# Optimization experiments

Hardware: AMD Instinct MI355X
Metric: run time of the kernel (lower is better)

Reference implementation:

```python
import jax, jax.numpy as jnp
import numpy as np

SCENE = (60, 36, 60)          # int(4.8/0.08), int(2.88/0.08), int(4.8/0.08)
VOX = 0.08
DS = 4
IMG_W, IMG_H = 640, 480
N_VOX = SCENE[0] * SCENE[1] * SCENE[2]

def _voxel_grid():
    gx, gy, gz = np.meshgrid(np.arange(SCENE[0]), np.arange(SCENE[1]), np.arange(SCENE[2]), indexing='ij')
    return np.stack([gx.ravel(), gy.ravel(), gz.ravel()], axis=1).astype(np.float32)  # [N,3]

_GRID = jnp.asarray(_voxel_grid())


def setup_inputs() -> dict:
    key = jax.random.key(0)
    x2d = jax.random.normal(jax.random.fold_in(key, 0), (512, IMG_H // DS, IMG_W // DS), dtype=jnp.float32)
    inv_cam_pose = jnp.eye(4, dtype=jnp.float32)
    vox_origin = jnp.array([-2.4, -2.4, 0.1], dtype=jnp.float32)
    cam_k = jnp.array([[518.8579, 0.0, 320.0], [0.0, 518.8579, 240.0], [0.0, 0.0, 1.0]], dtype=jnp.float32)
    old_voxel_indices = jax.random.randint(jax.random.fold_in(key, 1), (1000, 3), 0, 60)
    old_image_indices = jax.random.randint(jax.random.fold_in(key, 2), (1000, 2), 0, 480)
    return {"x2d": x2d, "inv_cam_pose": inv_cam_pose, "vox_origin": vox_origin, "cam_k": cam_k,
            "old_voxel_indices": old_voxel_indices, "old_image_indices": old_image_indices, "fliplr": 0}


def reference(x2d, inv_cam_pose, vox_origin, cam_k, old_voxel_indices, old_image_indices, fliplr):
    # old_voxel_indices / old_image_indices are unused in the original forward.
    c, h, w = x2d.shape
    grid = _GRID                                        # [N,3] voxel integer coords (float)
    pts_world2 = grid * VOX + 0.5 * VOX                 # voxel centers
    # axis swap: world (x, z, y) then shift by origin
    pts_world = jnp.stack([pts_world2[:, 0], pts_world2[:, 2], pts_world2[:, 1]], axis=1) + vox_origin[None, :]
    homo = jnp.concatenate([pts_world, jnp.ones((pts_world.shape[0], 1), pts_world.dtype)], axis=1)
    pts_cam = homo @ inv_cam_pose.T                     # [N,4] camera frame
    in_front = pts_cam[:, 2] > 0
    pts_img = pts_cam[:, :3] @ cam_k.T                  # [N,3]
    uv = jnp.round(pts_img[:, :2] / pts_img[:, 2:3])    # [N,2] = (x_col, y_row)
    in_frustum = (uv[:, 0] >= 0) & (uv[:, 0] < IMG_W) & (uv[:, 1] >= 0) & (uv[:, 1] < IMG_H)
    mask = in_front & in_frustum

    row, col = uv[:, 1], uv[:, 0]                       # torch.fliplr -> (y, x)
    if fliplr:
        col = IMG_W - 1 - col
    row = jnp.floor(row / DS)                           # // downsample
    col = jnp.floor(col / DS)
    lin_img = jnp.where(mask, (row * w + col), 0.0).astype(jnp.int32)  # safe gather index

    src = x2d.reshape(c, -1)
    feats = src[:, lin_img]                             # [c, N] gather

    lin_vox = (grid[:, 0] * (SCENE[1] * SCENE[2]) + grid[:, 1] * SCENE[2] + grid[:, 2]).astype(jnp.int32)
    lin_vox = jnp.where(mask, lin_vox, N_VOX)           # out-of-range -> dropped
    x3d = jnp.zeros((c, N_VOX), x2d.dtype).at[:, lin_vox].set(feats, mode='drop')
    return x3d.reshape(c, SCENE[0], SCENE[1], SCENE[2])
```

## Files before the change

kernel.cpp:

```cpp
#include <hip/hip_runtime.h>

#define NVOX 129600
#define NCH  512
#define IMH  120
#define IMW  160
#define NPIX (IMH * IMW)
#define LSTRIDE 161
#define PLANE_LDS (IMH * LSTRIDE)

typedef float vfloat4 __attribute__((ext_vector_type(4)));

__device__ __forceinline__ int project_voxel_pad(
    int v, const float* __restrict__ pose, const float* __restrict__ origin,
    const float* __restrict__ camk, int flip)
{
    int gx = v / 2160;
    int r  = v - gx * 2160;
    int gy = r / 60;
    int gz = r - gy * 60;
    float wx = gx * 0.08f + 0.04f + origin[0];
    float wy = gz * 0.08f + 0.04f + origin[1];
    float wz = gy * 0.08f + 0.04f + origin[2];
    float cx = pose[0]*wx + pose[1]*wy + pose[2]*wz  + pose[3];
    float cy = pose[4]*wx + pose[5]*wy + pose[6]*wz  + pose[7];
    float cz = pose[8]*wx + pose[9]*wy + pose[10]*wz + pose[11];
    float ix = camk[0]*cx + camk[1]*cy + camk[2]*cz;
    float iy = camk[3]*cx + camk[4]*cy + camk[5]*cz;
    float iz = camk[6]*cx + camk[7]*cy + camk[8]*cz;
    float u  = rintf(ix / iz);
    float vv = rintf(iy / iz);
    bool ok = (cz > 0.0f) && (u >= 0.0f) && (u < 640.0f)
                          && (vv >= 0.0f) && (vv < 480.0f);
    if (!ok) return -1;
    float colf = flip ? (639.0f - u) : u;
    return (((int)vv) >> 2) * LSTRIDE + (((int)colf) >> 2);
}

__global__ __launch_bounds__(256) void proj_kernel(
    int* __restrict__ lin,
    const float* __restrict__ pose, const float* __restrict__ origin,
    const float* __restrict__ camk, const int* __restrict__ fliplr)
{
    int v = blockIdx.x * 256 + threadIdx.x;
    if (v < NVOX)
        lin[v] = project_voxel_pad(v, pose, origin, camk, fliplr[0]);
}

__global__ __launch_bounds__(1024, 8) void chan_kernel(
    const float* __restrict__ x2d, const int* __restrict__ lin,
    float* __restrict__ out)
{
    __shared__ float plane[PLANE_LDS];
    int c = blockIdx.x;
    int t = threadIdx.x;

    const float4* src4 = reinterpret_cast<const float4*>(x2d)
                       + (size_t)c * (NPIX / 4);
#pragma unroll
    for (int i = 0; i < 5; ++i) {
        int p4 = i * 1024 + t;
        if (p4 < NPIX / 4) {
            float4 val = src4[p4];
            int p   = p4 * 4;
            int row = p / IMW;
            int col = p - row * IMW;
            float* d = &plane[row * LSTRIDE + col];
            d[0] = val.x; d[1] = val.y; d[2] = val.z; d[3] = val.w;
        }
    }
    __syncthreads();

    const int4* lin4 = reinterpret_cast<const int4*>(lin);
    vfloat4* out4 = reinterpret_cast<vfloat4*>(out) + (size_t)c * (NVOX / 4);
#pragma unroll 4
    for (int i = 0; i < 32; ++i) {
        int g = i * 1024 + t;
        if (g < NVOX / 4) {
            int4 l = lin4[g];
            vfloat4 o;
            o.x = (l.x >= 0) ? plane[l.x] : 0.0f;
            o.y = (l.y >= 0) ? plane[l.y] : 0.0f;
            o.z = (l.z >= 0) ? plane[l.z] : 0.0f;
            o.w = (l.w >= 0) ? plane[l.w] : 0.0f;
            __builtin_nontemporal_store(o, &out4[g]);
        }
    }
}

__global__ __launch_bounds__(256) void fused_kernel(
    const float* __restrict__ x2d, const float* __restrict__ pose,
    const float* __restrict__ origin, const float* __restrict__ camk,
    const int* __restrict__ fliplr, float* __restrict__ out)
{
    long tid = (long)blockIdx.x * blockDim.x + threadIdx.x;
    int g  = (int)(tid % 32400);
    int cg = (int)(tid / 32400);
    if (cg >= 64) return;
    int v0 = g * 4;
    int linv[4];
#pragma unroll
    for (int i = 0; i < 4; ++i) {
        int lp = project_voxel_pad(v0 + i, pose, origin, camk, fliplr[0]);
        linv[i] = (lp >= 0) ? (lp - lp / LSTRIDE) : -1;
    }
    int ch0 = cg * 8;
#pragma unroll
    for (int cc = 0; cc < 8; ++cc) {
        int ch = ch0 + cc;
        const float* s = x2d + (size_t)ch * NPIX;
        float4 o;
        o.x = (linv[0] >= 0) ? s[linv[0]] : 0.0f;
        o.y = (linv[1] >= 0) ? s[linv[1]] : 0.0f;
        o.z = (linv[2] >= 0) ? s[linv[2]] : 0.0f;
        o.w = (linv[3] >= 0) ? s[linv[3]] : 0.0f;
        *reinterpret_cast<float4*>(out + (size_t)ch * NVOX + v0) = o;
    }
}

extern "C" void kernel_launch(void* const* d_in, const int* in_sizes, int n_in,
                              void* d_out, int out_size, void* d_ws, size_t ws_size,
                              hipStream_t stream) {
    const float* x2d    = (const float*)d_in[0];
    const float* pose   = (const float*)d_in[1];
    const float* origin = (const float*)d_in[2];
    const float* camk   = (const float*)d_in[3];
    const int*   flip   = (const int*)d_in[6];
    float*       out    = (float*)d_out;

    const size_t lin_bytes = (size_t)NVOX * sizeof(int);
    if (ws_size >= lin_bytes) {
        int* linb = (int*)d_ws;
        proj_kernel<<<dim3((NVOX + 255) / 256), dim3(256), 0, stream>>>(
            linb, pose, origin, camk, flip);
        chan_kernel<<<dim3(NCH), dim3(1024), 0, stream>>>(x2d, linb, out);
    } else {
        fused_kernel<<<dim3(8100), dim3(256), 0, stream>>>(
            x2d, pose, origin, camk, flip, out);
    }
}
```

Before: 65.52 us.

## Process two channels per block with interleaved LDS plane and 16-bit indices

The channel kernel now handles two channels per block. It interleaves both planes into LDS as float2 pairs so that one LDS read serves both outputs, and it reuses each index load across two channels. Projection indices are stored as 16-bit values, which halves index traffic, and the plane loads use nontemporal loads. In exchange LDS use doubles to about 155KB per block and only 256 blocks are launched, so occupancy and wave-level parallelism drop.

New measurement: 63.66 us. 2.8% less time.

```diff
diff --git a/kernel.cpp b/kernel.cpp
--- a/kernel.cpp
+++ b/kernel.cpp
@@ -5,14 +5,16 @@
 #define IMH  120
 #define IMW  160
 #define NPIX (IMH * IMW)
-#define LSTRIDE 161
-#define PLANE_LDS (IMH * LSTRIDE)
+#define LSTR2 162
+#define PLANE2 (IMH * LSTR2)
 
 typedef float vfloat4 __attribute__((ext_vector_type(4)));
+typedef float vfloat2 __attribute__((ext_vector_type(2)));
+typedef unsigned short vushort4 __attribute__((ext_vector_type(4)));
 
-__device__ __forceinline__ int project_voxel_pad(
+__device__ __forceinline__ int project_voxel_s(
     int v, const float* __restrict__ pose, const float* __restrict__ origin,
-    const float* __restrict__ camk, int flip)
+    const float* __restrict__ camk, int flip, int stride)
 {
     int gx = v / 2160;
     int r  = v - gx * 2160;
@@ -33,56 +35,71 @@
                           && (vv >= 0.0f) && (vv < 480.0f);
     if (!ok) return -1;
     float colf = flip ? (639.0f - u) : u;
-    return (((int)vv) >> 2) * LSTRIDE + (((int)colf) >> 2);
+    return (((int)vv) >> 2) * stride + (((int)colf) >> 2);
 }
 
 __global__ __launch_bounds__(256) void proj_kernel(
-    int* __restrict__ lin,
+    unsigned short* __restrict__ lin16,
     const float* __restrict__ pose, const float* __restrict__ origin,
     const float* __restrict__ camk, const int* __restrict__ fliplr)
 {
     int v = blockIdx.x * 256 + threadIdx.x;
-    if (v < NVOX)
-        lin[v] = project_voxel_pad(v, pose, origin, camk, fliplr[0]);
+    if (v < NVOX) {
+        int l = project_voxel_s(v, pose, origin, camk, fliplr[0], LSTR2);
+        lin16[v] = (l >= 0) ? (unsigned short)l : (unsigned short)0xFFFF;
+    }
 }
 
-__global__ __launch_bounds__(1024, 8) void chan_kernel(
-    const float* __restrict__ x2d, const int* __restrict__ lin,
+__global__ __launch_bounds__(1024, 1) void chan2_kernel(
+    const float* __restrict__ x2d, const unsigned short* __restrict__ lin16,
     float* __restrict__ out)
 {
-    __shared__ float plane[PLANE_LDS];
-    int c = blockIdx.x;
+    __shared__ vfloat2 plane[PLANE2];
+    int b = blockIdx.x;
     int t = threadIdx.x;
+    int c0 = b * 2;
 
-    const float4* src4 = reinterpret_cast<const float4*>(x2d)
-                       + (size_t)c * (NPIX / 4);
+    const vfloat4* srcA = reinterpret_cast<const vfloat4*>(
+        x2d + (size_t)c0 * NPIX);
+    const vfloat4* srcB = reinterpret_cast<const vfloat4*>(
+        x2d + (size_t)(c0 + 1) * NPIX);
 #pragma unroll
     for (int i = 0; i < 5; ++i) {
-        int p4 = i * 1024 + t;
-        if (p4 < NPIX / 4) {
-            float4 val = src4[p4];
-            int p   = p4 * 4;
+        int j = i * 1024 + t;
+        if (j < NPIX / 4) {
+            vfloat4 a  = __builtin_nontemporal_load(&srcA[j]);
+            vfloat4 b4 = __builtin_nontemporal_load(&srcB[j]);
+            int p   = j * 4;
             int row = p / IMW;
             int col = p - row * IMW;
-            float* d = &plane[row * LSTRIDE + col];
-            d[0] = val.x; d[1] = val.y; d[2] = val.z; d[3] = val.w;
+            int idx = row * LSTR2 + col;
+            vfloat4 w0 = {a.x, b4.x, a.y, b4.y};
+            vfloat4 w1 = {a.z, b4.z, a.w, b4.w};
+            *reinterpret_cast<vfloat4*>(&plane[idx])     = w0;
+            *reinterpret_cast<vfloat4*>(&plane[idx + 2]) = w1;
         }
     }
     __syncthreads();
 
-    const int4* lin4 = reinterpret_cast<const int4*>(lin);
-    vfloat4* out4 = reinterpret_cast<vfloat4*>(out) + (size_t)c * (NVOX / 4);
+    vfloat4* outA = reinterpret_cast<vfloat4*>(out + (size_t)c0 * NVOX);
+    vfloat4* outB = reinterpret_cast<vfloat4*>(out + (size_t)(c0 + 1) * NVOX);
 #pragma unroll 4
     for (int i = 0; i < 32; ++i) {
         int g = i * 1024 + t;
         if (g < NVOX / 4) {
-            int4 l = lin4[g];
-            vfloat4 o;
-            o.x = (l.x >= 0) ? plane[l.x] : 0.0f;
-            o.y = (l.y >= 0) ? plane[l.y] : 0.0f;
-            o.z = (l.z >= 0) ? plane[l.z] : 0.0f;
-            o.w = (l.w >= 0) ? plane[l.w] : 0.0f;
-            __builtin_nontemporal_store(o, &out4[g]);
+            vushort4 l4 = *reinterpret_cast<const vushort4*>(lin16 + g * 4);
+            bool m0 = l4.x != 0xFFFFu, m1 = l4.y != 0xFFFFu,
+                 m2 = l4.z != 0xFFFFu, m3 = l4.w != 0xFFFFu;
+            vfloat2 v0 = plane[m0 ? l4.x : 0];
+            vfloat2 v1 = plane[m1 ? l4.y : 0];
+            vfloat2 v2 = plane[m2 ? l4.z : 0];
+            vfloat2 v3 = plane[m3 ? l4.w : 0];
+            vfloat4 oA = { m0 ? v0.x : 0.0f, m1 ? v1.x : 0.0f,
+                           m2 ? v2.x : 0.0f, m3 ? v3.x : 0.0f };
+            vfloat4 oB = { m0 ? v0.y : 0.0f, m1 ? v1.y : 0.0f,
+                           m2 ? v2.y : 0.0f, m3 ? v3.y : 0.0f };
+            __builtin_nontemporal_store(oA, &outA[g]);
+            __builtin_nontemporal_store(oB, &outB[g]);
         }
     }
 }
@@ -99,10 +116,8 @@
     int v0 = g * 4;
     int linv[4];
 #pragma unroll
-    for (int i = 0; i < 4; ++i) {
-        int lp = project_voxel_pad(v0 + i, pose, origin, camk, fliplr[0]);
-        linv[i] = (lp >= 0) ? (lp - lp / LSTRIDE) : -1;
-    }
+    for (int i = 0; i < 4; ++i)
+        linv[i] = project_voxel_s(v0 + i, pose, origin, camk, fliplr[0], IMW);
     int ch0 = cg * 8;
 #pragma unroll
     for (int cc = 0; cc < 8; ++cc) {
@@ -127,12 +142,13 @@
     const int*   flip   = (const int*)d_in[6];
     float*       out    = (float*)d_out;
 
-    const size_t lin_bytes = (size_t)NVOX * sizeof(int);
+    const size_t lin_bytes = (size_t)NVOX * sizeof(unsigned short);
     if (ws_size >= lin_bytes) {
-        int* linb = (int*)d_ws;
+        unsigned short* lin16 = (unsigned short*)d_ws;
         proj_kernel<<<dim3((NVOX + 255) / 256), dim3(256), 0, stream>>>(
-            linb, pose, origin, camk, flip);
-        chan_kernel<<<dim3(NCH), dim3(1024), 0, stream>>>(x2d, linb, out);
+            lin16, pose, origin, camk, flip);
+        chan2_kernel<<<dim3(NCH / 2), dim3(1024), 0, stream>>>(
+            x2d, lin16, out);
     } else {
         fused_kernel<<<dim3(8100), dim3(256), 0, stream>>>(
             x2d, pose, origin, camk, flip, out);
```
